# Performance work log

Measured on AMD Instinct MI355X. Metric: run time of the kernel, lower is better.

Reference implementation:

```python
import jax, jax.numpy as jnp
import numpy as np

B, H, S, D = 2, 16, 2048, 64

def setup_inputs() -> dict:
    key = jax.random.key(0)
    kq, kk, kv, km = jax.random.split(key, 4)
    Q = jax.random.normal(kq, (B, H, S, D), dtype=jnp.float32)
    K = jax.random.normal(kk, (B, H, S, D), dtype=jnp.float32)
    V = jax.random.normal(kv, (B, H, S, D), dtype=jnp.float32)
    # padding-style boolean mask, broadcast over heads; True = masked out
    attn_mask = jax.random.randint(km, (B, 1, S, S), 0, 2).astype(jnp.bool_)
    return {"Q": Q, "K": K, "V": V, "attn_mask": attn_mask}

def reference(Q, K, V, attn_mask):
    d = Q.shape[-1]
    scale = 1.0 / np.sqrt(d).astype(np.float32)
    # [B,H,S,S] scores
    scores = jnp.einsum('bhqd,bhkd->bhqk', Q, K) * scale
    scores = jnp.where(attn_mask, jnp.float32(-1e9), scores)
    attn = jax.nn.softmax(scores, axis=-1)
    context = jnp.einsum('bhqk,bhkd->bhqd', attn, V)
    return context
```

## Files before the change

kernel.cpp:

```cpp
#include <hip/hip_runtime.h>

#define B_ 2
#define H_ 16
#define S_ 2048
#define D_ 64
#define BK 32
#define NKT (S_ / BK)
#define QSCALE 0.18033688011112042f
#define MFIX 16.0f

#define KSD 36
#define VTD 18
#define KS_SZ (BK * KSD)
#define VT_SZ (D_ * VTD)

typedef __attribute__((ext_vector_type(4))) float  float4v;
typedef __attribute__((ext_vector_type(2))) _Float16 half2v;
typedef __attribute__((ext_vector_type(4))) _Float16 half4v;
typedef __attribute__((ext_vector_type(8))) _Float16 half8v;
typedef __attribute__((ext_vector_type(2))) __fp16 fp16x2;
typedef __attribute__((ext_vector_type(2))) unsigned uint2v;

union H2U { half2v h; fp16x2 g; unsigned u; };
union H4U { half4v h4; half2v h2[2]; fp16x2 g2[2]; uint2v u2; };
union H8U { half8v h8; fp16x2 g2[4]; };

__device__ __forceinline__ unsigned pkh(float a, float b) {
    H2U c; c.g = __builtin_amdgcn_cvt_pkrtz(a, b);
    return c.u;
}
__device__ __forceinline__ float fexp2(float x) {
#if __has_builtin(__builtin_amdgcn_exp2f)
    return __builtin_amdgcn_exp2f(x);
#else
    return exp2f(x);
#endif
}

__device__ __forceinline__ void wg_barrier() {
    asm volatile("s_waitcnt lgkmcnt(0)\n\ts_barrier" ::: "memory");
}

struct Stage { float4 k0, k1, va, vb; };

__device__ __forceinline__ void stage_load(const float* __restrict__ Kg,
                                           const float* __restrict__ Vg,
                                           int kk, int dd, Stage& s) {
    s.k0 = *(const float4*)(Kg + (size_t)kk * D_ + dd);
    s.k1 = *(const float4*)(Kg + (size_t)(kk + 16) * D_ + dd);
    s.va = *(const float4*)(Vg + (size_t)(2 * kk) * D_ + dd);
    s.vb = *(const float4*)(Vg + (size_t)(2 * kk + 1) * D_ + dd);
}

__device__ __forceinline__ void stage_store(unsigned* KsB, unsigned* VtB,
                                            int kwa, int kwb, const int* vw,
                                            const Stage& s) {
    *(uint2v*)&KsB[kwa] = (uint2v){ pkh(s.k0.x, s.k0.y), pkh(s.k0.z, s.k0.w) };
    *(uint2v*)&KsB[kwb] = (uint2v){ pkh(s.k1.x, s.k1.y), pkh(s.k1.z, s.k1.w) };
    VtB[vw[0]] = pkh(s.va.x, s.vb.x);
    VtB[vw[1]] = pkh(s.va.y, s.vb.y);
    VtB[vw[2]] = pkh(s.va.z, s.vb.z);
    VtB[vw[3]] = pkh(s.va.w, s.vb.w);
}

__device__ __forceinline__ float4 mask2bias(int4 m) {
    float4 r;
    r.x = m.x ? -1e9f : -MFIX;  r.y = m.y ? -1e9f : -MFIX;
    r.z = m.z ? -1e9f : -MFIX;  r.w = m.w ? -1e9f : -MFIX;
    return r;
}

__global__ __launch_bounds__(256, 4)
void attn_flash_st(const float* __restrict__ Q, const float* __restrict__ K,
                   const float* __restrict__ V, const int* __restrict__ mask,
                   float* __restrict__ out)
{
    __shared__ unsigned KsAll[2 * KS_SZ];
    __shared__ unsigned VtAll[2 * VT_SZ];

    const int tid  = threadIdx.x;
    const int lane = tid & 63;
    const int l15  = lane & 15;
    const int quad = lane >> 4;
    const int wave = tid >> 6;
    const int bh   = blockIdx.y;
    const int b    = bh / H_;
    const int qbase = blockIdx.x * 64 + wave * 16;
    const size_t qkv = (size_t)bh * S_ * D_;

    half8v qf[2];
    {
        const float* qrow = Q + qkv + (size_t)(qbase + l15) * D_ + quad * 8;
        #pragma unroll
        for (int dc = 0; dc < 2; ++dc) {
            float4 f0 = *(const float4*)(qrow + dc * 32);
            float4 f1 = *(const float4*)(qrow + dc * 32 + 4);
            H8U u;
            u.g2[0] = __builtin_amdgcn_cvt_pkrtz(f0.x * QSCALE, f0.y * QSCALE);
            u.g2[1] = __builtin_amdgcn_cvt_pkrtz(f0.z * QSCALE, f0.w * QSCALE);
            u.g2[2] = __builtin_amdgcn_cvt_pkrtz(f1.x * QSCALE, f1.y * QSCALE);
            u.g2[3] = __builtin_amdgcn_cvt_pkrtz(f1.z * QSCALE, f1.w * QSCALE);
            qf[dc] = u.h8;
        }
    }

    const int kk = tid >> 4;
    const int dd = (tid & 15) * 4;
    const int kwa = kk * KSD + (tid & 15) * 2;
    const int kwb = (kk + 16) * KSD + (tid & 15) * 2;
    int vw[4];
    #pragma unroll
    for (int m = 0; m < 4; ++m)
        vw[m] = (dd + m) * VTD + (kk ^ ((((dd + m) >> 4) & 3) << 1));

    int kroff[2][2];
    #pragma unroll
    for (int t = 0; t < 2; ++t)
        #pragma unroll
        for (int dc = 0; dc < 2; ++dc)
            kroff[t][dc] = (t * 16 + l15) * KSD + dc * 16 + quad * 4;
    int vrd[4][2];
    #pragma unroll
    for (int nb = 0; nb < 4; ++nb)
        #pragma unroll
        for (int t = 0; t < 2; ++t)
            vrd[nb][t] = (nb * 16 + l15) * VTD + ((t * 8 + quad * 2) ^ ((nb & 3) << 1));

    const int* mrow0 = mask + (size_t)b * S_ * S_ + (size_t)(qbase + l15) * S_ + quad * 4;

    float l_lane = 0.0f;
    float4v o[4];
    #pragma unroll
    for (int nb = 0; nb < 4; ++nb) o[nb] = (float4v){0.f, 0.f, 0.f, 0.f};

    const float* Kg0 = K + qkv;
    const float* Vg0 = V + qkv;

    Stage sA, sB;
    stage_load(Kg0, Vg0, kk, dd, sA);
    stage_store(KsAll, VtAll, kwa, kwb, vw, sA);
    stage_load(Kg0 + BK * D_, Vg0 + BK * D_, kk, dd, sB);
    float4 mk0 = mask2bias(*(const int4*)(mrow0));
    float4 mk1 = mask2bias(*(const int4*)(mrow0 + 16));
    wg_barrier();

    auto iter = [&](int kt, const unsigned* KsB, const unsigned* VtB,
                    unsigned* KsN, unsigned* VtN, Stage& pre, Stage& sto) {
        const int ktn = (kt + 2 < NKT) ? kt + 2 : NKT - 1;
        stage_load(Kg0 + (size_t)ktn * BK * D_, Vg0 + (size_t)ktn * BK * D_, kk, dd, pre);
        const int mtn = (kt + 1 < NKT) ? kt + 1 : NKT - 1;
        const int* mnext = mrow0 + (size_t)mtn * BK;
        const float4 nm0 = mask2bias(*(const int4*)(mnext));
        const float4 nm1 = mask2bias(*(const int4*)(mnext + 16));

        float4v st0 = (float4v){0.f,0.f,0.f,0.f}, st1 = st0;
        {
            half8v kf;
            kf = *(const half8v*)&KsB[kroff[0][0]];
            st0 = __builtin_amdgcn_mfma_f32_16x16x32_f16(kf, qf[0], st0, 0, 0, 0);
            kf = *(const half8v*)&KsB[kroff[0][1]];
            st0 = __builtin_amdgcn_mfma_f32_16x16x32_f16(kf, qf[1], st0, 0, 0, 0);
            kf = *(const half8v*)&KsB[kroff[1][0]];
            st1 = __builtin_amdgcn_mfma_f32_16x16x32_f16(kf, qf[0], st1, 0, 0, 0);
            kf = *(const half8v*)&KsB[kroff[1][1]];
            st1 = __builtin_amdgcn_mfma_f32_16x16x32_f16(kf, qf[1], st1, 0, 0, 0);
        }

        float4v p0, p1;
        p0.x = fexp2(st0.x + mk0.x); p0.y = fexp2(st0.y + mk0.y);
        p0.z = fexp2(st0.z + mk0.z); p0.w = fexp2(st0.w + mk0.w);
        p1.x = fexp2(st1.x + mk1.x); p1.y = fexp2(st1.y + mk1.y);
        p1.z = fexp2(st1.z + mk1.z); p1.w = fexp2(st1.w + mk1.w);

        l_lane += ((p0.x + p0.y) + (p0.z + p0.w)) +
                  ((p1.x + p1.y) + (p1.z + p1.w));

        H4U pf0u, pf1u;
        pf0u.g2[0] = __builtin_amdgcn_cvt_pkrtz(p0.x, p0.y);
        pf0u.g2[1] = __builtin_amdgcn_cvt_pkrtz(p0.z, p0.w);
        pf1u.g2[0] = __builtin_amdgcn_cvt_pkrtz(p1.x, p1.y);
        pf1u.g2[1] = __builtin_amdgcn_cvt_pkrtz(p1.z, p1.w);

        #pragma unroll
        for (int nb = 0; nb < 4; ++nb) {
            H4U vf;
            vf.u2 = *(const uint2v*)&VtB[vrd[nb][0]];
            o[nb] = __builtin_amdgcn_mfma_f32_16x16x16f16(vf.h4, pf0u.h4, o[nb], 0, 0, 0);
            vf.u2 = *(const uint2v*)&VtB[vrd[nb][1]];
            o[nb] = __builtin_amdgcn_mfma_f32_16x16x16f16(vf.h4, pf1u.h4, o[nb], 0, 0, 0);
        }

        stage_store(KsN, VtN, kwa, kwb, vw, sto);
        wg_barrier();
        mk0 = nm0; mk1 = nm1;
    };

    #pragma unroll 1
    for (int kt2 = 0; kt2 < NKT; kt2 += 2) {
        iter(kt2,     KsAll,         VtAll,         (unsigned*)KsAll + KS_SZ, (unsigned*)VtAll + VT_SZ, sA, sB);
        iter(kt2 + 1, KsAll + KS_SZ, VtAll + VT_SZ, (unsigned*)KsAll,         (unsigned*)VtAll,         sB, sA);
    }

    float ls = l_lane;
    ls += __shfl_xor(ls, 16, 64);
    ls += __shfl_xor(ls, 32, 64);
    const float inv = 1.0f / ls;

    float* orow = out + qkv + (size_t)(qbase + l15) * D_ + quad * 4;
    #pragma unroll
    for (int nb = 0; nb < 4; ++nb) {
        float4 ov = { o[nb].x * inv, o[nb].y * inv, o[nb].z * inv, o[nb].w * inv };
        *(float4*)(orow + nb * 16) = ov;
    }
}

extern "C" void kernel_launch(void* const* d_in, const int* in_sizes, int n_in,
                              void* d_out, int out_size, void* d_ws, size_t ws_size,
                              hipStream_t stream) {
    const float* Q    = (const float*)d_in[0];
    const float* K    = (const float*)d_in[1];
    const float* V    = (const float*)d_in[2];
    const int*   mask = (const int*)d_in[3];
    float* out = (float*)d_out;

    dim3 grid(S_ / 64, B_ * H_);
    dim3 block(256);
    attn_flash_st<<<grid, block, 0, stream>>>(Q, K, V, mask, out);
}
```

Before: 196.2 us.

## Double key tile to 64 and simplify prefetch to single-stage register buffer

Raises the key/value tile per iteration from 32 to 64 rows. This halves the number of workgroup barriers and loop iterations and gives the MFMA chains more independent work per step. Global prefetch now runs one tile ahead with a single register stage instead of two. Mask values are loaded in the current iteration rather than one ahead, which may expose more global load latency. Register pressure also rises from the larger staging struct.

Measured after the change: 204.8 us. 4.4% more time.

```diff
diff --git a/kernel.cpp b/kernel.cpp
--- a/kernel.cpp
+++ b/kernel.cpp
@@ -4,13 +4,13 @@
 #define H_ 16
 #define S_ 2048
 #define D_ 64
-#define BK 32
+#define BK 64
 #define NKT (S_ / BK)
 #define QSCALE 0.18033688011112042f
 #define MFIX 16.0f
 
 #define KSD 36
-#define VTD 18
+#define VTD 34
 #define KS_SZ (BK * KSD)
 #define VT_SZ (D_ * VTD)
 
@@ -41,33 +41,36 @@
     asm volatile("s_waitcnt lgkmcnt(0)\n\ts_barrier" ::: "memory");
 }
 
-struct Stage { float4 k0, k1, va, vb; };
+struct Stage { float4 k0, k1, k2, k3, va0, vb0, va1, vb1; };
 
 __device__ __forceinline__ void stage_load(const float* __restrict__ Kg,
                                            const float* __restrict__ Vg,
                                            int kk, int dd, Stage& s) {
-    s.k0 = *(const float4*)(Kg + (size_t)kk * D_ + dd);
-    s.k1 = *(const float4*)(Kg + (size_t)(kk + 16) * D_ + dd);
-    s.va = *(const float4*)(Vg + (size_t)(2 * kk) * D_ + dd);
-    s.vb = *(const float4*)(Vg + (size_t)(2 * kk + 1) * D_ + dd);
+    s.k0 = *(const float4*)(Kg + (size_t)(kk      ) * D_ + dd);
+    s.k1 = *(const float4*)(Kg + (size_t)(kk + 16 ) * D_ + dd);
+    s.k2 = *(const float4*)(Kg + (size_t)(kk + 32 ) * D_ + dd);
+    s.k3 = *(const float4*)(Kg + (size_t)(kk + 48 ) * D_ + dd);
+    s.va0 = *(const float4*)(Vg + (size_t)(2 * kk     ) * D_ + dd);
+    s.vb0 = *(const float4*)(Vg + (size_t)(2 * kk + 1 ) * D_ + dd);
+    s.va1 = *(const float4*)(Vg + (size_t)(2 * kk + 32) * D_ + dd);
+    s.vb1 = *(const float4*)(Vg + (size_t)(2 * kk + 33) * D_ + dd);
 }
 
 __device__ __forceinline__ void stage_store(unsigned* KsB, unsigned* VtB,
-                                            int kwa, int kwb, const int* vw,
+                                            int kwa, const int* vw,
                                             const Stage& s) {
-    *(uint2v*)&KsB[kwa] = (uint2v){ pkh(s.k0.x, s.k0.y), pkh(s.k0.z, s.k0.w) };
-    *(uint2v*)&KsB[kwb] = (uint2v){ pkh(s.k1.x, s.k1.y), pkh(s.k1.z, s.k1.w) };
-    VtB[vw[0]] = pkh(s.va.x, s.vb.x);
-    VtB[vw[1]] = pkh(s.va.y, s.vb.y);
-    VtB[vw[2]] = pkh(s.va.z, s.vb.z);
-    VtB[vw[3]] = pkh(s.va.w, s.vb.w);
-}
-
-__device__ __forceinline__ float4 mask2bias(int4 m) {
-    float4 r;
-    r.x = m.x ? -1e9f : -MFIX;  r.y = m.y ? -1e9f : -MFIX;
-    r.z = m.z ? -1e9f : -MFIX;  r.w = m.w ? -1e9f : -MFIX;
-    return r;
+    *(uint2v*)&KsB[kwa           ] = (uint2v){ pkh(s.k0.x, s.k0.y), pkh(s.k0.z, s.k0.w) };
+    *(uint2v*)&KsB[kwa + 16 * KSD] = (uint2v){ pkh(s.k1.x, s.k1.y), pkh(s.k1.z, s.k1.w) };
+    *(uint2v*)&KsB[kwa + 32 * KSD] = (uint2v){ pkh(s.k2.x, s.k2.y), pkh(s.k2.z, s.k2.w) };
+    *(uint2v*)&KsB[kwa + 48 * KSD] = (uint2v){ pkh(s.k3.x, s.k3.y), pkh(s.k3.z, s.k3.w) };
+    VtB[vw[0]     ] = pkh(s.va0.x, s.vb0.x);
+    VtB[vw[0] + 16] = pkh(s.va1.x, s.vb1.x);
+    VtB[vw[1]     ] = pkh(s.va0.y, s.vb0.y);
+    VtB[vw[1] + 16] = pkh(s.va1.y, s.vb1.y);
+    VtB[vw[2]     ] = pkh(s.va0.z, s.vb0.z);
+    VtB[vw[2] + 16] = pkh(s.va1.z, s.vb1.z);
+    VtB[vw[3]     ] = pkh(s.va0.w, s.vb0.w);
+    VtB[vw[3] + 16] = pkh(s.va1.w, s.vb1.w);
 }
 
 __global__ __launch_bounds__(256, 4)
@@ -107,24 +110,16 @@
     const int kk = tid >> 4;
     const int dd = (tid & 15) * 4;
     const int kwa = kk * KSD + (tid & 15) * 2;
-    const int kwb = (kk + 16) * KSD + (tid & 15) * 2;
     int vw[4];
     #pragma unroll
     for (int m = 0; m < 4; ++m)
         vw[m] = (dd + m) * VTD + (kk ^ ((((dd + m) >> 4) & 3) << 1));
 
-    int kroff[2][2];
-    #pragma unroll
-    for (int t = 0; t < 2; ++t)
-        #pragma unroll
-        for (int dc = 0; dc < 2; ++dc)
-            kroff[t][dc] = (t * 16 + l15) * KSD + dc * 16 + quad * 4;
-    int vrd[4][2];
+    const int kbase = l15 * KSD + quad * 4;
+    int vbase[4];
     #pragma unroll
     for (int nb = 0; nb < 4; ++nb)
-        #pragma unroll
-        for (int t = 0; t < 2; ++t)
-            vrd[nb][t] = (nb * 16 + l15) * VTD + ((t * 8 + quad * 2) ^ ((nb & 3) << 1));
+        vbase[nb] = (nb * 16 + l15) * VTD + ((quad * 2) ^ (nb << 1));
 
     const int* mrow0 = mask + (size_t)b * S_ * S_ + (size_t)(qbase + l15) * S_ + quad * 4;
 
@@ -136,69 +131,65 @@
     const float* Kg0 = K + qkv;
     const float* Vg0 = V + qkv;
 
-    Stage sA, sB;
-    stage_load(Kg0, Vg0, kk, dd, sA);
-    stage_store(KsAll, VtAll, kwa, kwb, vw, sA);
-    stage_load(Kg0 + BK * D_, Vg0 + BK * D_, kk, dd, sB);
-    float4 mk0 = mask2bias(*(const int4*)(mrow0));
-    float4 mk1 = mask2bias(*(const int4*)(mrow0 + 16));
+    Stage sg;
+    stage_load(Kg0, Vg0, kk, dd, sg);
+    stage_store(KsAll, VtAll, kwa, vw, sg);
     wg_barrier();
 
     auto iter = [&](int kt, const unsigned* KsB, const unsigned* VtB,
-                    unsigned* KsN, unsigned* VtN, Stage& pre, Stage& sto) {
-        const int ktn = (kt + 2 < NKT) ? kt + 2 : NKT - 1;
-        stage_load(Kg0 + (size_t)ktn * BK * D_, Vg0 + (size_t)ktn * BK * D_, kk, dd, pre);
-        const int mtn = (kt + 1 < NKT) ? kt + 1 : NKT - 1;
-        const int* mnext = mrow0 + (size_t)mtn * BK;
-        const float4 nm0 = mask2bias(*(const int4*)(mnext));
-        const float4 nm1 = mask2bias(*(const int4*)(mnext + 16));
-
-        float4v st0 = (float4v){0.f,0.f,0.f,0.f}, st1 = st0;
-        {
+                    unsigned* KsN, unsigned* VtN) {
+        const int ktn = (kt + 1 < NKT) ? kt + 1 : NKT - 1;
+        stage_load(Kg0 + (size_t)ktn * BK * D_, Vg0 + (size_t)ktn * BK * D_, kk, dd, sg);
+
+        const int* mrow = mrow0 + (size_t)kt * BK;
+        int4 mk[4];
+        #pragma unroll
+        for (int t = 0; t < 4; ++t) mk[t] = *(const int4*)(mrow + t * 16);
+
+        float4v st[4];
+        #pragma unroll
+        for (int t = 0; t < 4; ++t) {
             half8v kf;
-            kf = *(const half8v*)&KsB[kroff[0][0]];
-            st0 = __builtin_amdgcn_mfma_f32_16x16x32_f16(kf, qf[0], st0, 0, 0, 0);
-            kf = *(const half8v*)&KsB[kroff[0][1]];
-            st0 = __builtin_amdgcn_mfma_f32_16x16x32_f16(kf, qf[1], st0, 0, 0, 0);
-            kf = *(const half8v*)&KsB[kroff[1][0]];
-            st1 = __builtin_amdgcn_mfma_f32_16x16x32_f16(kf, qf[0], st1, 0, 0, 0);
-            kf = *(const half8v*)&KsB[kroff[1][1]];
-            st1 = __builtin_amdgcn_mfma_f32_16x16x32_f16(kf, qf[1], st1, 0, 0, 0);
-        }
-
-        float4v p0, p1;
-        p0.x = fexp2(st0.x + mk0.x); p0.y = fexp2(st0.y + mk0.y);
-        p0.z = fexp2(st0.z + mk0.z); p0.w = fexp2(st0.w + mk0.w);
-        p1.x = fexp2(st1.x + mk1.x); p1.y = fexp2(st1.y + mk1.y);
-        p1.z = fexp2(st1.z + mk1.z); p1.w = fexp2(st1.w + mk1.w);
-
-        l_lane += ((p0.x + p0.y) + (p0.z + p0.w)) +
-                  ((p1.x + p1.y) + (p1.z + p1.w));
-
-        H4U pf0u, pf1u;
-        pf0u.g2[0] = __builtin_amdgcn_cvt_pkrtz(p0.x, p0.y);
-        pf0u.g2[1] = __builtin_amdgcn_cvt_pkrtz(p0.z, p0.w);
-        pf1u.g2[0] = __builtin_amdgcn_cvt_pkrtz(p1.x, p1.y);
-        pf1u.g2[1] = __builtin_amdgcn_cvt_pkrtz(p1.z, p1.w);
+            kf = *(const half8v*)&KsB[kbase + t * 16 * KSD];
+            float4v acc = (float4v){0.f, 0.f, 0.f, 0.f};
+            acc = __builtin_amdgcn_mfma_f32_16x16x32_f16(kf, qf[0], acc, 0, 0, 0);
+            kf = *(const half8v*)&KsB[kbase + t * 16 * KSD + 16];
+            st[t] = __builtin_amdgcn_mfma_f32_16x16x32_f16(kf, qf[1], acc, 0, 0, 0);
+        }
+
+        H4U pf[4];
+        float lacc = 0.0f;
+        #pragma unroll
+        for (int t = 0; t < 4; ++t) {
+            float4v p;
+            p.x = fexp2(st[t].x + (mk[t].x ? -1e9f : -MFIX));
+            p.y = fexp2(st[t].y + (mk[t].y ? -1e9f : -MFIX));
+            p.z = fexp2(st[t].z + (mk[t].z ? -1e9f : -MFIX));
+            p.w = fexp2(st[t].w + (mk[t].w ? -1e9f : -MFIX));
+            lacc += (p.x + p.y) + (p.z + p.w);
+            pf[t].g2[0] = __builtin_amdgcn_cvt_pkrtz(p.x, p.y);
+            pf[t].g2[1] = __builtin_amdgcn_cvt_pkrtz(p.z, p.w);
+        }
+        l_lane += lacc;
 
         #pragma unroll
         for (int nb = 0; nb < 4; ++nb) {
-            H4U vf;
-            vf.u2 = *(const uint2v*)&VtB[vrd[nb][0]];
-            o[nb] = __builtin_amdgcn_mfma_f32_16x16x16f16(vf.h4, pf0u.h4, o[nb], 0, 0, 0);
-            vf.u2 = *(const uint2v*)&VtB[vrd[nb][1]];
-            o[nb] = __builtin_amdgcn_mfma_f32_16x16x16f16(vf.h4, pf1u.h4, o[nb], 0, 0, 0);
-        }
-
-        stage_store(KsN, VtN, kwa, kwb, vw, sto);
+            #pragma unroll
+            for (int t = 0; t < 4; ++t) {
+                H4U vf;
+                vf.u2 = *(const uint2v*)&VtB[vbase[nb] + t * 8];
+                o[nb] = __builtin_amdgcn_mfma_f32_16x16x16f16(vf.h4, pf[t].h4, o[nb], 0, 0, 0);
+            }
+        }
+
+        stage_store(KsN, VtN, kwa, vw, sg);
         wg_barrier();
-        mk0 = nm0; mk1 = nm1;
     };
 
     #pragma unroll 1
     for (int kt2 = 0; kt2 < NKT; kt2 += 2) {
-        iter(kt2,     KsAll,         VtAll,         (unsigned*)KsAll + KS_SZ, (unsigned*)VtAll + VT_SZ, sA, sB);
-        iter(kt2 + 1, KsAll + KS_SZ, VtAll + VT_SZ, (unsigned*)KsAll,         (unsigned*)VtAll,         sB, sA);
+        iter(kt2,     KsAll,         VtAll,         (unsigned*)KsAll + KS_SZ, (unsigned*)VtAll + VT_SZ);
+        iter(kt2 + 1, KsAll + KS_SZ, VtAll + VT_SZ, (unsigned*)KsAll,         (unsigned*)VtAll);
     }
 
     float ls = l_lane;
```
